# Performance work log

Hardware: AMD Instinct MI355X
Metric: run time of the kernel (lower is better)

The kernel has to match this reference:

```python
import jax, jax.numpy as jnp
import numpy as np

NUM_HEADS = 16
ROPE_THETA = 10000.0


def _rope_angles(seq_len, head_dim, dtype):
    # lucidrains rotary_embedding_torch: freqs = theta^(-2i/d) for i in 0..d/2,
    # angles = pos * freq, then each angle repeated twice along last dim (interleaved pairs).
    inv_freq = 1.0 / (ROPE_THETA ** (jnp.arange(0, head_dim, 2, dtype=jnp.float32) / head_dim))
    angles = jnp.arange(seq_len, dtype=jnp.float32)[:, None] * inv_freq  # [N, D/2]
    return jnp.repeat(angles, 2, axis=-1).astype(dtype)  # [N, D]


def _rotate_half(t):
    # interleaved pairs: (x0, x1) -> (-x1, x0)
    t1 = t[..., ::2]
    t2 = t[..., 1::2]
    return jnp.stack([-t2, t1], axis=-1).reshape(t.shape)


def _apply_rope(t, cos, sin):
    # t: [B, H, N, D]; cos/sin: [N, D]
    return t * cos + _rotate_half(t) * sin


def setup_inputs() -> dict:
    key = jax.random.key(0)
    ks = jax.random.split(key, 5)
    B, N, C = 4, 1024, 1024
    return {
        "x": jax.random.normal(ks[0], (B, N, C), dtype=jnp.float32),
        "w_qkv": jax.random.normal(ks[1], (C, 3 * C), dtype=jnp.float32) * (C ** -0.5),
        "b_qkv": jax.random.normal(ks[2], (3 * C,), dtype=jnp.float32) * 0.02,
        "w_proj": jax.random.normal(ks[3], (C, C), dtype=jnp.float32) * (C ** -0.5),
        "b_proj": jax.random.normal(ks[4], (C,), dtype=jnp.float32) * 0.02,
    }


def reference(x, w_qkv, b_qkv, w_proj, b_proj):
    B, N, C = x.shape
    H = NUM_HEADS
    D = C // H

    qkv = x @ w_qkv + b_qkv  # [B, N, 3C]
    qkv = qkv.reshape(B, N, 3, H, D).transpose(2, 0, 3, 1, 4)  # [3, B, H, N, D]
    q, k, v = qkv[0], qkv[1], qkv[2]

    ang = _rope_angles(N, D, x.dtype)
    cos, sin = jnp.cos(ang), jnp.sin(ang)
    q = _apply_rope(q, cos, sin)
    k = _apply_rope(k, cos, sin)

    scale = D ** -0.5  # SDPA default scale
    scores = jnp.einsum("bhqd,bhkd->bhqk", q, k) * scale
    attn = jax.nn.softmax(scores, axis=-1)
    out = jnp.einsum("bhqk,bhkd->bhqd", attn, v)  # [B, H, N, D]

    out = out.transpose(0, 2, 1, 3).reshape(B, N, C)
    return out @ w_proj + b_proj
```

## Files before the change

### kernel.cpp

```cpp
#include <hip/hip_runtime.h>
#include <math.h>

#define BB 4
#define NN 1024
#define CC 1024
#define HH 16
#define DD 64
#define N3 3072

typedef __attribute__((ext_vector_type(8))) short bf16x8;
typedef __attribute__((ext_vector_type(8))) _Float16 f16x8;
typedef __attribute__((ext_vector_type(4))) _Float16 f16x4;
typedef __attribute__((ext_vector_type(4))) float f32x4;
typedef __attribute__((ext_vector_type(4))) unsigned int u32x4;
typedef __attribute__((ext_vector_type(2))) unsigned int u32x2;

struct ushort4_t { unsigned short x, y, z, w; };

static __device__ __forceinline__ unsigned short f2b(float f) {
    union { float f; unsigned int u; } v; v.f = f;
    unsigned int r = (v.u + 0x7fffu + ((v.u >> 16) & 1u)) >> 16;
    return (unsigned short)r;
}

static __device__ __forceinline__ void ldg_lds16(const void* g, void* l) {
    __builtin_amdgcn_global_load_lds(
        (const __attribute__((address_space(1))) unsigned int*)g,
        (__attribute__((address_space(3))) unsigned int*)l, 16, 0, 0);
}

__global__ __launch_bounds__(256) void prep(const float* __restrict__ x,
                                            const float* __restrict__ wq,
                                            const float* __restrict__ wp,
                                            _Float16* __restrict__ Xh,
                                            _Float16* __restrict__ Wqt,
                                            _Float16* __restrict__ Wpt,
                                            float* __restrict__ ct,
                                            float* __restrict__ st) {
    __shared__ __align__(16) _Float16 T[64][72];
    const int blk = blockIdx.x;
    const int t = threadIdx.x;
    if (blk < 4096) {
        int tid = blk * 256 + t;
        float4 v = ((const float4*)x)[tid];
        f16x4 o = {(_Float16)v.x, (_Float16)v.y, (_Float16)v.z, (_Float16)v.w};
        ((f16x4*)Xh)[tid] = o;
    } else if (blk < 5120) {
        const float* src; _Float16* dst; int ns, k0, n0;
        if (blk < 4864) {
            int idx = blk - 4096;
            k0 = (idx & 15) * 64; n0 = (idx >> 4) * 64;
            src = wq; dst = Wqt; ns = N3;
        } else {
            int idx = blk - 4864;
            k0 = (idx & 15) * 64; n0 = (idx >> 4) * 64;
            src = wp; dst = Wpt; ns = 1024;
        }
        {
            const int r  = t >> 2;
            const int cf = (t & 3) * 16;
            const float* sp = src + (size_t)(k0 + r) * ns + n0 + cf;
            float4 v0 = *(const float4*)(sp);
            float4 v1 = *(const float4*)(sp + 4);
            float4 v2 = *(const float4*)(sp + 8);
            float4 v3 = *(const float4*)(sp + 12);
            f16x8 a, b;
            a[0]=(_Float16)v0.x; a[1]=(_Float16)v0.y; a[2]=(_Float16)v0.z; a[3]=(_Float16)v0.w;
            a[4]=(_Float16)v1.x; a[5]=(_Float16)v1.y; a[6]=(_Float16)v1.z; a[7]=(_Float16)v1.w;
            b[0]=(_Float16)v2.x; b[1]=(_Float16)v2.y; b[2]=(_Float16)v2.z; b[3]=(_Float16)v2.w;
            b[4]=(_Float16)v3.x; b[5]=(_Float16)v3.y; b[6]=(_Float16)v3.z; b[7]=(_Float16)v3.w;
            *(f16x8*)&T[r][cf]     = a;
            *(f16x8*)&T[r][cf + 8] = b;
        }
        __syncthreads();
        {
            const int n  = t >> 2;
            const int kc = t & 3;
            f16x8 o0, o1;
            #pragma unroll
            for (int kk = 0; kk < 8; kk++) o0[kk] = T[kc * 16 + kk][n];
            #pragma unroll
            for (int kk = 0; kk < 8; kk++) o1[kk] = T[kc * 16 + 8 + kk][n];
            _Float16* dp = dst + (size_t)(n0 + n) * 1024 + k0 + kc * 16;
            *(f16x8*)dp       = o0;
            *(f16x8*)(dp + 8) = o1;
        }
    } else {
        int tid = (blk - 5120) * 256 + t;
        int n = tid >> 5, i = tid & 31;
        double ang = (double)n * exp2(-(double)i * (13.287712379549449 / 32.0));
        ct[tid] = (float)cos(ang);
        st[tid] = (float)sin(ang);
    }
}

template<int BM, int BN>
static __device__ __forceinline__ void gemm_body32(const char* gA, const char* gB,
                                                   int m0, int n0,
                                                   _Float16* As0, _Float16* As1,
                                                   _Float16* Bs0, _Float16* Bs1,
                                                   int tid, int ln, int qd,
                                                   int wm, int wn,
                                                   f32x4 (&acc)[BM / 32][BN / 32]) {
    constexpr int PA = BM / 64, PB = BN / 64, MR = BM / 32, NR = BN / 32;
    const int lrow = tid >> 2;
    const int lc   = tid & 3;
    const int swz  = (lc ^ (lrow & 3)) * 8;
    const int rsz  = (qd ^ (ln & 3)) * 8;

    u32x4 pa[PA], pb[PB];

    #pragma unroll
    for (int p = 0; p < PA; p++)
        pa[p] = *(const u32x4*)(gA + (size_t)(m0 + p * 64 + lrow) * 2048 + lc * 16);
    #pragma unroll
    for (int p = 0; p < PB; p++)
        pb[p] = *(const u32x4*)(gB + (size_t)(n0 + p * 64 + lrow) * 2048 + lc * 16);
    #pragma unroll
    for (int p = 0; p < PA; p++) *(u32x4*)&As0[(p * 64 + lrow) * 32 + swz] = pa[p];
    #pragma unroll
    for (int p = 0; p < PB; p++) *(u32x4*)&Bs0[(p * 64 + lrow) * 32 + swz] = pb[p];
    #pragma unroll
    for (int p = 0; p < PA; p++)
        pa[p] = *(const u32x4*)(gA + (size_t)(m0 + p * 64 + lrow) * 2048 + 64 + lc * 16);
    #pragma unroll
    for (int p = 0; p < PB; p++)
        pb[p] = *(const u32x4*)(gB + (size_t)(n0 + p * 64 + lrow) * 2048 + 64 + lc * 16);
    __syncthreads();

    #pragma unroll
    for (int t = 0; t < 32; t++) {
        const _Float16* Ac = (t & 1) ? As1 : As0;
        const _Float16* Bc = (t & 1) ? Bs1 : Bs0;

        f16x8 af[MR], bf[NR];
        #pragma unroll
        for (int i = 0; i < MR; i++)
            af[i] = *(const f16x8*)&Ac[(wm + i * 16 + ln) * 32 + rsz];
        #pragma unroll
        for (int j = 0; j < NR; j++)
            bf[j] = *(const f16x8*)&Bc[(wn + j * 16 + ln) * 32 + rsz];
        #pragma unroll
        for (int i = 0; i < MR; i++)
            #pragma unroll
            for (int j = 0; j < NR; j++)
                acc[i][j] = __builtin_amdgcn_mfma_f32_16x16x32_f16(af[i], bf[j],
                                                                   acc[i][j], 0, 0, 0);

        if (t < 31) {
            _Float16* An = (t & 1) ? As0 : As1;
            _Float16* Bn = (t & 1) ? Bs0 : Bs1;
            #pragma unroll
            for (int p = 0; p < PA; p++) *(u32x4*)&An[(p * 64 + lrow) * 32 + swz] = pa[p];
            #pragma unroll
            for (int p = 0; p < PB; p++) *(u32x4*)&Bn[(p * 64 + lrow) * 32 + swz] = pb[p];
            if (t < 30) {
                size_t ko = (size_t)(t + 2) * 64;
                #pragma unroll
                for (int p = 0; p < PA; p++)
                    pa[p] = *(const u32x4*)(gA + (size_t)(m0 + p * 64 + lrow) * 2048 + ko + lc * 16);
                #pragma unroll
                for (int p = 0; p < PB; p++)
                    pb[p] = *(const u32x4*)(gB + (size_t)(n0 + p * 64 + lrow) * 2048 + ko + lc * 16);
            }
        }
        __syncthreads();
    }
}

static __device__ __forceinline__ void gemm_body_pipe_n64(const char* gA, const char* gB,
                                                          int m0, int n0,
                                                          _Float16* As0, _Float16* As1,
                                                          _Float16* Bs0, _Float16* Bs1,
                                                          int tid, int ln, int qd,
                                                          int wm, int wn, f32x4 acc[4][2]) {
    const int lrow   = tid >> 3;
    const int lchunk = tid & 7;
    const int swz    = (lchunk ^ (lrow & 7)) * 8;

    u32x4 pa[4], pb[2];

    #pragma unroll
    for (int c = 0; c < 4; c++)
        pa[c] = *(const u32x4*)(gA + (size_t)(m0 + c * 32 + lrow) * 2048 + lchunk * 16);
    #pragma unroll
    for (int c = 0; c < 2; c++)
        pb[c] = *(const u32x4*)(gB + (size_t)(n0 + c * 32 + lrow) * 2048 + lchunk * 16);
    #pragma unroll
    for (int c = 0; c < 4; c++)
        *(u32x4*)&As0[(c * 32 + lrow) * 64 + swz] = pa[c];
    #pragma unroll
    for (int c = 0; c < 2; c++)
        *(u32x4*)&Bs0[(c * 32 + lrow) * 64 + swz] = pb[c];
    #pragma unroll
    for (int c = 0; c < 4; c++)
        pa[c] = *(const u32x4*)(gA + (size_t)(m0 + c * 32 + lrow) * 2048 + 128 + lchunk * 16);
    #pragma unroll
    for (int c = 0; c < 2; c++)
        pb[c] = *(const u32x4*)(gB + (size_t)(n0 + c * 32 + lrow) * 2048 + 128 + lchunk * 16);
    __syncthreads();

    #pragma unroll
    for (int t = 0; t < 16; t++) {
        const _Float16* Ac = (t & 1) ? As1 : As0;
        const _Float16* Bc = (t & 1) ? Bs1 : Bs0;

        #pragma unroll
        for (int kc = 0; kc < 2; kc++) {
            f16x8 af[4], bf[2];
            #pragma unroll
            for (int i = 0; i < 4; i++)
                af[i] = *(const f16x8*)&Ac[(wm + i * 16 + ln) * 64 +
                                           (((kc * 4 + qd) ^ (ln & 7)) * 8)];
            #pragma unroll
            for (int j = 0; j < 2; j++)
                bf[j] = *(const f16x8*)&Bc[(wn + j * 16 + ln) * 64 +
                                           (((kc * 4 + qd) ^ (ln & 7)) * 8)];
            #pragma unroll
            for (int i = 0; i < 4; i++)
                #pragma unroll
                for (int j = 0; j < 2; j++)
                    acc[i][j] = __builtin_amdgcn_mfma_f32_16x16x32_f16(af[i], bf[j],
                                                                       acc[i][j], 0, 0, 0);
        }

        if (t < 15) {
            _Float16* An = (t & 1) ? As0 : As1;
            _Float16* Bn = (t & 1) ? Bs0 : Bs1;
            #pragma unroll
            for (int c = 0; c < 4; c++)
                *(u32x4*)&An[(c * 32 + lrow) * 64 + swz] = pa[c];
            #pragma unroll
            for (int c = 0; c < 2; c++)
                *(u32x4*)&Bn[(c * 32 + lrow) * 64 + swz] = pb[c];
            if (t < 14) {
                size_t ko = (size_t)(t + 2) * 128;
                #pragma unroll
                for (int c = 0; c < 4; c++)
                    pa[c] = *(const u32x4*)(gA + (size_t)(m0 + c * 32 + lrow) * 2048 + ko + lchunk * 16);
                #pragma unroll
                for (int c = 0; c < 2; c++)
                    pb[c] = *(const u32x4*)(gB + (size_t)(n0 + c * 32 + lrow) * 2048 + ko + lchunk * 16);
            }
        }
        __syncthreads();
    }
}

__global__ __launch_bounds__(256, 3) void qkv_mfma(const _Float16* __restrict__ Ah,
                                                   const _Float16* __restrict__ Bt,
                                                   const float* __restrict__ bias,
                                                   const float* __restrict__ cost,
                                                   const float* __restrict__ sint,
                                                   unsigned short* __restrict__ Q,
                                                   unsigned short* __restrict__ K,
                                                   unsigned short* __restrict__ Vtg) {
    __shared__ __align__(16) _Float16 As[2][128 * 32];
    __shared__ __align__(16) _Float16 Bs[2][128 * 32];
    const int t = threadIdx.x;
    const int lane = t & 63;
    const int w = t >> 6;
    const int ln = lane & 15, qd = lane >> 4;
    const int n0 = blockIdx.x * 128;
    const int m0 = blockIdx.y * 128;
    const int wm = (w >> 1) * 64, wn = (w & 1) * 64;

    f32x4 acc[4][4];
    #pragma unroll
    for (int i = 0; i < 4; i++)
        #pragma unroll
        for (int j = 0; j < 4; j++) acc[i][j] = (f32x4){0.f, 0.f, 0.f, 0.f};

    gemm_body32<128, 128>((const char*)Ah, (const char*)Bt, m0, n0,
                          As[0], As[1], Bs[0], Bs[1], t, ln, qd, wm, wn, acc);

    const int s = n0 >> 10;
    const int h = ((n0 + wn) >> 6) & 15;
    if (s < 2) {
        unsigned short* dst = (s == 0) ? Q : K;
        const float sc0 = (s == 0) ? 0.125f : 1.0f;
        #pragma unroll
        for (int i = 0; i < 4; i++) {
            #pragma unroll
            for (int reg = 0; reg < 4; reg++) {
                int row = m0 + wm + i * 16 + qd * 4 + reg;
                int b = row >> 10, n = row & 1023;
                size_t obase = (((size_t)(b * HH + h)) * NN + n) * DD;
                #pragma unroll
                for (int j = 0; j < 4; j++) {
                    int d = j * 16 + ln;
                    float v = acc[i][j][reg] + bias[n0 + wn + d];
                    float pv = __shfl_xor(v, 1);
                    float cs = cost[n * 32 + (d >> 1)];
                    float sn = sint[n * 32 + (d >> 1)];
                    float outv = ((d & 1) ? (v * cs + pv * sn) : (v * cs - pv * sn)) * sc0;
                    dst[obase + d] = f2b(outv);
                }
            }
        }
    } else {
        #pragma unroll
        for (int i = 0; i < 4; i++) {
            int row0 = m0 + wm + i * 16 + qd * 4;
            int b = row0 >> 10, n = row0 & 1023;
            size_t tbase = ((size_t)(b * HH + h)) * DD * NN + n;
            #pragma unroll
            for (int j = 0; j < 4; j++) {
                int d = j * 16 + ln;
                float bb = bias[n0 + wn + d];
                ushort4_t pk;
                pk.x = f2b(acc[i][j][0] + bb);
                pk.y = f2b(acc[i][j][1] + bb);
                pk.z = f2b(acc[i][j][2] + bb);
                pk.w = f2b(acc[i][j][3] + bb);
                *(ushort4_t*)&Vtg[tbase + (size_t)d * NN] = pk;
            }
        }
    }
}

__global__ __launch_bounds__(256) void attn_flash(const unsigned short* __restrict__ Qb,
                                                  const unsigned short* __restrict__ Kb,
                                                  const unsigned short* __restrict__ Vtg,
                                                  _Float16* __restrict__ AO) {
    __shared__ __align__(16) unsigned short Ks[3][64 * 64];
    __shared__ __align__(16) unsigned short Vt[2][64 * 64];
    __shared__ __align__(16) unsigned short Ps[4][32 * 64];

    const int t    = threadIdx.x;
    const int lane = t & 63;
    const int w    = t >> 6;
    const int ln   = lane & 15;
    const int qd   = lane >> 4;
    const int bq   = blockIdx.x;
    const int h    = blockIdx.y;
    const int b    = blockIdx.z;
    const size_t base = (size_t)(b * HH + h) * NN * DD;
    const char* Kc = (const char*)(Kb + base);
    const char* Vc = (const char*)(Vtg + base);
    const int xorc = ((lane & 7) ^ (lane >> 3)) * 16;
    const int r8   = lane >> 3;
    const int wrow = w * 16;

    bf16x8 qf[2][2];
    #pragma unroll
    for (int g = 0; g < 2; g++) {
        const unsigned short* qp = Qb + base +
            (size_t)(bq * 128 + w * 32 + g * 16 + ln) * DD + qd * 8;
        qf[g][0] = *(const bf16x8*)qp;
        qf[g][1] = *(const bf16x8*)(qp + 32);
    }

    f32x4 o[2][5];
    #pragma unroll
    for (int g = 0; g < 2; g++)
        #pragma unroll
        for (int x = 0; x < 5; x++) o[g][x] = (f32x4){0.f, 0.f, 0.f, 0.f};

    bf16x8 onesf;
    #pragma unroll
    for (int x = 0; x < 8; x++) onesf[x] = (short)0x3F80;

    #pragma unroll
    for (int tile = 0; tile < 3; tile++)
        #pragma unroll
        for (int c = 0; c < 2; c++) {
            int rr = wrow + c * 8 + r8;
            ldg_lds16(Kc + (size_t)(tile * 64 + rr) * 128 + xorc,
                      &Ks[tile][(wrow + c * 8) * 64]);
        }
    #pragma unroll
    for (int tile = 0; tile < 2; tile++)
        #pragma unroll
        for (int c = 0; c < 2; c++) {
            int rr = wrow + c * 8 + r8;
            ldg_lds16(Vc + (size_t)rr * 2048 + (size_t)tile * 128 + xorc,
                      &Vt[tile][(wrow + c * 8) * 64]);
        }
    __syncthreads();

    f32x4 scur[2][4];
    {
        const unsigned short* KsB = Ks[0];
        #pragma unroll
        for (int j = 0; j < 4; j++) {
            bf16x8 k0f = *(const bf16x8*)&KsB[(ln + 16 * j) * 64 + ((qd ^ (ln & 7)) * 8)];
            bf16x8 k1f = *(const bf16x8*)&KsB[(ln + 16 * j) * 64 + (((4 + qd) ^ (ln & 7)) * 8)];
            #pragma unroll
            for (int g = 0; g < 2; g++) {
                f32x4 sj = {0.f, 0.f, 0.f, 0.f};
                sj = __builtin_amdgcn_mfma_f32_16x16x32_bf16(k0f, qf[g][0], sj, 0, 0, 0);
                sj = __builtin_amdgcn_mfma_f32_16x16x32_bf16(k1f, qf[g][1], sj, 0, 0, 0);
                scur[g][j] = sj;
            }
        }
    }

    const float C1 = 1.44269504f;
    const float C0 = -16.0f * 1.44269504f;
    const int swp = 2 * (ln & 7);

    #pragma unroll
    for (int tt = 0; tt < 16; tt++) {
        f32x4 snext[2][4];
        if (tt < 15) {
            const unsigned short* KsB = Ks[(tt + 1) % 3];
            #pragma unroll
            for (int j = 0; j < 4; j++) {
                bf16x8 k0f = *(const bf16x8*)&KsB[(ln + 16 * j) * 64 + ((qd ^ (ln & 7)) * 8)];
                bf16x8 k1f = *(const bf16x8*)&KsB[(ln + 16 * j) * 64 + (((4 + qd) ^ (ln & 7)) * 8)];
                #pragma unroll
                for (int g = 0; g < 2; g++) {
                    f32x4 sj = {0.f, 0.f, 0.f, 0.f};
                    sj = __builtin_amdgcn_mfma_f32_16x16x32_bf16(k0f, qf[g][0], sj, 0, 0, 0);
                    sj = __builtin_amdgcn_mfma_f32_16x16x32_bf16(k1f, qf[g][1], sj, 0, 0, 0);
                    snext[g][j] = sj;
                }
            }
        }

        unsigned short* PsB = &Ps[w][0];
        #pragma unroll
        for (int g = 0; g < 2; g++) {
            char* rowp = (char*)PsB + (g * 16 + ln) * 128;
            #pragma unroll
            for (int j = 0; j < 4; j++) {
                float p0 = exp2f(fmaf(scur[g][j][0], C1, C0));
                float p1 = exp2f(fmaf(scur[g][j][1], C1, C0));
                float p2 = exp2f(fmaf(scur[g][j][2], C1, C0));
                float p3 = exp2f(fmaf(scur[g][j][3], C1, C0));
                unsigned int lo, hi;
                asm("v_cvt_pk_bf16_f32 %0, %1, %2" : "=v"(lo) : "v"(p0), "v"(p1));
                asm("v_cvt_pk_bf16_f32 %0, %1, %2" : "=v"(hi) : "v"(p2), "v"(p3));
                u32x2 pk; pk[0] = lo; pk[1] = hi;
                *(u32x2*)(rowp + (((4 * j + qd) ^ swp) * 8)) = pk;
            }
        }

        {
            const unsigned short* VtB = Vt[tt & 1];
            bf16x8 pf[2][2];
            #pragma unroll
            for (int g = 0; g < 2; g++) {
                pf[g][0] = *(const bf16x8*)&PsB[(g * 16 + ln) * 64 + ((qd ^ (ln & 7)) * 8)];
                pf[g][1] = *(const bf16x8*)&PsB[(g * 16 + ln) * 64 + (((4 + qd) ^ (ln & 7)) * 8)];
            }
            #pragma unroll
            for (int j = 0; j < 4; j++) {
                bf16x8 v0f = *(const bf16x8*)&VtB[(ln + 16 * j) * 64 + ((qd ^ (ln & 7)) * 8)];
                bf16x8 v1f = *(const bf16x8*)&VtB[(ln + 16 * j) * 64 + (((4 + qd) ^ (ln & 7)) * 8)];
                #pragma unroll
                for (int g = 0; g < 2; g++) {
                    o[g][j] = __builtin_amdgcn_mfma_f32_16x16x32_bf16(pf[g][0], v0f, o[g][j], 0, 0, 0);
                    o[g][j] = __builtin_amdgcn_mfma_f32_16x16x32_bf16(pf[g][1], v1f, o[g][j], 0, 0, 0);
                }
            }
            #pragma unroll
            for (int g = 0; g < 2; g++) {
                o[g][4] = __builtin_amdgcn_mfma_f32_16x16x32_bf16(pf[g][0], onesf, o[g][4], 0, 0, 0);
                o[g][4] = __builtin_amdgcn_mfma_f32_16x16x32_bf16(pf[g][1], onesf, o[g][4], 0, 0, 0);
            }
        }

        __syncthreads();

        if (tt <= 12) {
            int tile = tt + 3;
            #pragma unroll
            for (int c = 0; c < 2; c++) {
                int rr = wrow + c * 8 + r8;
                ldg_lds16(Kc + (size_t)(tile * 64 + rr) * 128 + xorc,
                          &Ks[tt % 3][(wrow + c * 8) * 64]);
            }
        }
        if (tt <= 13) {
            int tile = tt + 2;
            #pragma unroll
            for (int c = 0; c < 2; c++) {
                int rr = wrow + c * 8 + r8;
                ldg_lds16(Vc + (size_t)rr * 2048 + (size_t)tile * 128 + xorc,
                          &Vt[tt & 1][(wrow + c * 8) * 64]);
            }
        }

        #pragma unroll
        for (int g = 0; g < 2; g++)
            #pragma unroll
            for (int j = 0; j < 4; j++) scur[g][j] = snext[g][j];
    }

    #pragma unroll
    for (int g = 0; g < 2; g++)
        #pragma unroll
        for (int r = 0; r < 4; r++) {
            float inv = 1.0f / o[g][4][r];
            int q = bq * 128 + w * 32 + g * 16 + qd * 4 + r;
            _Float16* op = AO + (((size_t)b * NN + q) * HH + h) * DD + ln;
            op[0]  = (_Float16)(o[g][0][r] * inv);
            op[16] = (_Float16)(o[g][1][r] * inv);
            op[32] = (_Float16)(o[g][2][r] * inv);
            op[48] = (_Float16)(o[g][3][r] * inv);
        }
}

__global__ __launch_bounds__(256) void proj_mfma(const _Float16* __restrict__ Ah,
                                                 const _Float16* __restrict__ Bt,
                                                 const float* __restrict__ bias,
                                                 float* __restrict__ out) {
    __shared__ __align__(16) _Float16 As[2][128 * 64];
    __shared__ __align__(16) _Float16 Bs[2][64 * 64];
    const int t = threadIdx.x;
    const int lane = t & 63;
    const int w = t >> 6;
    const int ln = lane & 15, qd = lane >> 4;
    const int n0 = blockIdx.x * 64;
    const int m0 = blockIdx.y * 128;
    const int wm = (w >> 1) * 64, wn = (w & 1) * 32;

    f32x4 acc[4][2];
    #pragma unroll
    for (int i = 0; i < 4; i++)
        #pragma unroll
        for (int j = 0; j < 2; j++) acc[i][j] = (f32x4){0.f, 0.f, 0.f, 0.f};

    gemm_body_pipe_n64((const char*)Ah, (const char*)Bt, m0, n0,
                       As[0], As[1], Bs[0], Bs[1], t, ln, qd, wm, wn, acc);

    #pragma unroll
    for (int i = 0; i < 4; i++) {
        #pragma unroll
        for (int reg = 0; reg < 4; reg++) {
            int row = m0 + wm + i * 16 + qd * 4 + reg;
            #pragma unroll
            for (int j = 0; j < 2; j++) {
                int col = n0 + wn + j * 16 + ln;
                out[(size_t)row * 1024 + col] = acc[i][j][reg] + bias[col];
            }
        }
    }
}

extern "C" void kernel_launch(void* const* d_in, const int* in_sizes, int n_in,
                              void* d_out, int out_size, void* d_ws, size_t ws_size,
                              hipStream_t stream) {
    const float* x      = (const float*)d_in[0];
    const float* w_qkv  = (const float*)d_in[1];
    const float* b_qkv  = (const float*)d_in[2];
    const float* w_proj = (const float*)d_in[3];
    const float* b_proj = (const float*)d_in[4];
    float* out = (float*)d_out;

    char* ws = (char*)d_ws;
    _Float16* Xh   = (_Float16*)(ws);
    _Float16* Wqt  = (_Float16*)(ws + (8u << 20));
    _Float16* Wpt  = (_Float16*)(ws + (14u << 20));
    unsigned short* Q  = (unsigned short*)(ws + (16u << 20));
    unsigned short* K  = (unsigned short*)(ws + (24u << 20));
    unsigned short* Vt = (unsigned short*)(ws + (32u << 20));
    _Float16* AOh  = (_Float16*)(ws + (40u << 20));
    float* cost    = (float*)(ws + (48u << 20));
    float* sint    = (float*)(ws + (48u << 20) + (128u << 10));

    prep<<<5248, 256, 0, stream>>>(x, w_qkv, w_proj, Xh, Wqt, Wpt, cost, sint);
    qkv_mfma<<<dim3(24, 32), 256, 0, stream>>>(Xh, Wqt, b_qkv, cost, sint, Q, K, Vt);
    attn_flash<<<dim3(8, 16, 4), 256, 0, stream>>>(Q, K, Vt, AOh);
    proj_mfma<<<dim3(16, 32), 256, 0, stream>>>(AOh, Wpt, b_proj, out);
}
```

Before: 178.8 us.

## Rewrite QKV GEMM with 256x256 tiles and 4-stage direct-to-LDS pipeline

Replaces the register-staged double-buffered 128x128 QKV GEMM with a 512-thread, 256x256 tile kernel. Global loads now go straight into LDS through global_load_lds across a 4-slot ring, with explicit vmcnt/lgkmcnt waits, raw s_barrier, and setprio around the MFMA bursts. The aim is more operand reuse per block and better overlap of loads with compute. In exchange it uses much more LDS and more registers (128 accumulators per thread), and launches only 192 blocks, which could leave CUs idle and relies on hand-written wait counts being correct.

Result: no change. 177.0 us (-1.0%).

```diff
diff --git a/kernel.cpp b/kernel.cpp
--- a/kernel.cpp
+++ b/kernel.cpp
@@ -28,6 +28,14 @@
         (const __attribute__((address_space(1))) unsigned int*)g,
         (__attribute__((address_space(3))) unsigned int*)l, 16, 0, 0);
 }
+
+static __device__ __forceinline__ void barx()  { asm volatile("s_barrier" ::: "memory"); }
+static __device__ __forceinline__ void wlg0()  { asm volatile("s_waitcnt lgkmcnt(0)" ::: "memory");
+                                                 __builtin_amdgcn_sched_barrier(0); }
+static __device__ __forceinline__ void wvm8()  { asm volatile("s_waitcnt vmcnt(8)" ::: "memory"); }
+static __device__ __forceinline__ void wvm4()  { asm volatile("s_waitcnt vmcnt(4)" ::: "memory"); }
+static __device__ __forceinline__ void wvm0()  { asm volatile("s_waitcnt vmcnt(0)" ::: "memory"); }
+static __device__ __forceinline__ void wnone() {}
 
 __global__ __launch_bounds__(256) void prep(const float* __restrict__ x,
                                             const float* __restrict__ wq,
@@ -94,160 +102,7 @@
     }
 }
 
-template<int BM, int BN>
-static __device__ __forceinline__ void gemm_body32(const char* gA, const char* gB,
-                                                   int m0, int n0,
-                                                   _Float16* As0, _Float16* As1,
-                                                   _Float16* Bs0, _Float16* Bs1,
-                                                   int tid, int ln, int qd,
-                                                   int wm, int wn,
-                                                   f32x4 (&acc)[BM / 32][BN / 32]) {
-    constexpr int PA = BM / 64, PB = BN / 64, MR = BM / 32, NR = BN / 32;
-    const int lrow = tid >> 2;
-    const int lc   = tid & 3;
-    const int swz  = (lc ^ (lrow & 3)) * 8;
-    const int rsz  = (qd ^ (ln & 3)) * 8;
-
-    u32x4 pa[PA], pb[PB];
-
-    #pragma unroll
-    for (int p = 0; p < PA; p++)
-        pa[p] = *(const u32x4*)(gA + (size_t)(m0 + p * 64 + lrow) * 2048 + lc * 16);
-    #pragma unroll
-    for (int p = 0; p < PB; p++)
-        pb[p] = *(const u32x4*)(gB + (size_t)(n0 + p * 64 + lrow) * 2048 + lc * 16);
-    #pragma unroll
-    for (int p = 0; p < PA; p++) *(u32x4*)&As0[(p * 64 + lrow) * 32 + swz] = pa[p];
-    #pragma unroll
-    for (int p = 0; p < PB; p++) *(u32x4*)&Bs0[(p * 64 + lrow) * 32 + swz] = pb[p];
-    #pragma unroll
-    for (int p = 0; p < PA; p++)
-        pa[p] = *(const u32x4*)(gA + (size_t)(m0 + p * 64 + lrow) * 2048 + 64 + lc * 16);
-    #pragma unroll
-    for (int p = 0; p < PB; p++)
-        pb[p] = *(const u32x4*)(gB + (size_t)(n0 + p * 64 + lrow) * 2048 + 64 + lc * 16);
-    __syncthreads();
-
-    #pragma unroll
-    for (int t = 0; t < 32; t++) {
-        const _Float16* Ac = (t & 1) ? As1 : As0;
-        const _Float16* Bc = (t & 1) ? Bs1 : Bs0;
-
-        f16x8 af[MR], bf[NR];
-        #pragma unroll
-        for (int i = 0; i < MR; i++)
-            af[i] = *(const f16x8*)&Ac[(wm + i * 16 + ln) * 32 + rsz];
-        #pragma unroll
-        for (int j = 0; j < NR; j++)
-            bf[j] = *(const f16x8*)&Bc[(wn + j * 16 + ln) * 32 + rsz];
-        #pragma unroll
-        for (int i = 0; i < MR; i++)
-            #pragma unroll
-            for (int j = 0; j < NR; j++)
-                acc[i][j] = __builtin_amdgcn_mfma_f32_16x16x32_f16(af[i], bf[j],
-                                                                   acc[i][j], 0, 0, 0);
-
-        if (t < 31) {
-            _Float16* An = (t & 1) ? As0 : As1;
-            _Float16* Bn = (t & 1) ? Bs0 : Bs1;
-            #pragma unroll
-            for (int p = 0; p < PA; p++) *(u32x4*)&An[(p * 64 + lrow) * 32 + swz] = pa[p];
-            #pragma unroll
-            for (int p = 0; p < PB; p++) *(u32x4*)&Bn[(p * 64 + lrow) * 32 + swz] = pb[p];
-            if (t < 30) {
-                size_t ko = (size_t)(t + 2) * 64;
-                #pragma unroll
-                for (int p = 0; p < PA; p++)
-                    pa[p] = *(const u32x4*)(gA + (size_t)(m0 + p * 64 + lrow) * 2048 + ko + lc * 16);
-                #pragma unroll
-                for (int p = 0; p < PB; p++)
-                    pb[p] = *(const u32x4*)(gB + (size_t)(n0 + p * 64 + lrow) * 2048 + ko + lc * 16);
-            }
-        }
-        __syncthreads();
-    }
-}
-
-static __device__ __forceinline__ void gemm_body_pipe_n64(const char* gA, const char* gB,
-                                                          int m0, int n0,
-                                                          _Float16* As0, _Float16* As1,
-                                                          _Float16* Bs0, _Float16* Bs1,
-                                                          int tid, int ln, int qd,
-                                                          int wm, int wn, f32x4 acc[4][2]) {
-    const int lrow   = tid >> 3;
-    const int lchunk = tid & 7;
-    const int swz    = (lchunk ^ (lrow & 7)) * 8;
-
-    u32x4 pa[4], pb[2];
-
-    #pragma unroll
-    for (int c = 0; c < 4; c++)
-        pa[c] = *(const u32x4*)(gA + (size_t)(m0 + c * 32 + lrow) * 2048 + lchunk * 16);
-    #pragma unroll
-    for (int c = 0; c < 2; c++)
-        pb[c] = *(const u32x4*)(gB + (size_t)(n0 + c * 32 + lrow) * 2048 + lchunk * 16);
-    #pragma unroll
-    for (int c = 0; c < 4; c++)
-        *(u32x4*)&As0[(c * 32 + lrow) * 64 + swz] = pa[c];
-    #pragma unroll
-    for (int c = 0; c < 2; c++)
-        *(u32x4*)&Bs0[(c * 32 + lrow) * 64 + swz] = pb[c];
-    #pragma unroll
-    for (int c = 0; c < 4; c++)
-        pa[c] = *(const u32x4*)(gA + (size_t)(m0 + c * 32 + lrow) * 2048 + 128 + lchunk * 16);
-    #pragma unroll
-    for (int c = 0; c < 2; c++)
-        pb[c] = *(const u32x4*)(gB + (size_t)(n0 + c * 32 + lrow) * 2048 + 128 + lchunk * 16);
-    __syncthreads();
-
-    #pragma unroll
-    for (int t = 0; t < 16; t++) {
-        const _Float16* Ac = (t & 1) ? As1 : As0;
-        const _Float16* Bc = (t & 1) ? Bs1 : Bs0;
-
-        #pragma unroll
-        for (int kc = 0; kc < 2; kc++) {
-            f16x8 af[4], bf[2];
-            #pragma unroll
-            for (int i = 0; i < 4; i++)
-                af[i] = *(const f16x8*)&Ac[(wm + i * 16 + ln) * 64 +
-                                           (((kc * 4 + qd) ^ (ln & 7)) * 8)];
-            #pragma unroll
-            for (int j = 0; j < 2; j++)
-                bf[j] = *(const f16x8*)&Bc[(wn + j * 16 + ln) * 64 +
-                                           (((kc * 4 + qd) ^ (ln & 7)) * 8)];
-            #pragma unroll
-            for (int i = 0; i < 4; i++)
-                #pragma unroll
-                for (int j = 0; j < 2; j++)
-                    acc[i][j] = __builtin_amdgcn_mfma_f32_16x16x32_f16(af[i], bf[j],
-                                                                       acc[i][j], 0, 0, 0);
-        }
-
-        if (t < 15) {
-            _Float16* An = (t & 1) ? As0 : As1;
-            _Float16* Bn = (t & 1) ? Bs0 : Bs1;
-            #pragma unroll
-            for (int c = 0; c < 4; c++)
-                *(u32x4*)&An[(c * 32 + lrow) * 64 + swz] = pa[c];
-            #pragma unroll
-            for (int c = 0; c < 2; c++)
-                *(u32x4*)&Bn[(c * 32 + lrow) * 64 + swz] = pb[c];
-            if (t < 14) {
-                size_t ko = (size_t)(t + 2) * 128;
-                #pragma unroll
-                for (int c = 0; c < 4; c++)
-                    pa[c] = *(const u32x4*)(gA + (size_t)(m0 + c * 32 + lrow) * 2048 + ko + lchunk * 16);
-                #pragma unroll
-                for (int c = 0; c < 2; c++)
-                    pb[c] = *(const u32x4*)(gB + (size_t)(n0 + c * 32 + lrow) * 2048 + ko + lchunk * 16);
-            }
-        }
-        __syncthreads();
-    }
-}
-
-__global__ __launch_bounds__(256, 3) void qkv_mfma(const _Float16* __restrict__ Ah,
+__global__ __launch_bounds__(512, 2) void qkv_mfma(const _Float16* __restrict__ Ah,
                                                    const _Float16* __restrict__ Bt,
                                                    const float* __restrict__ bias,
                                                    const float* __restrict__ cost,
@@ -255,32 +110,103 @@
                                                    unsigned short* __restrict__ Q,
                                                    unsigned short* __restrict__ K,
                                                    unsigned short* __restrict__ Vtg) {
-    __shared__ __align__(16) _Float16 As[2][128 * 32];
-    __shared__ __align__(16) _Float16 Bs[2][128 * 32];
-    const int t = threadIdx.x;
+    __shared__ __align__(16) _Float16 LA[4][128 * 64];
+    __shared__ __align__(16) _Float16 LB[4][128 * 64];
+
+    const int t    = threadIdx.x;
     const int lane = t & 63;
-    const int w = t >> 6;
-    const int ln = lane & 15, qd = lane >> 4;
-    const int n0 = blockIdx.x * 128;
-    const int m0 = blockIdx.y * 128;
-    const int wm = (w >> 1) * 64, wn = (w & 1) * 64;
-
-    f32x4 acc[4][4];
-    #pragma unroll
-    for (int i = 0; i < 4; i++)
+    const int w    = t >> 6;
+    const int ln   = lane & 15, qd = lane >> 4;
+    const int n0   = blockIdx.x * 256;
+    const int m0   = blockIdx.y * 256;
+    const int wm   = (w >> 2) * 128;
+    const int wn   = (w & 3) * 64;
+
+    const int L0 = t >> 3, hc0 = (t & 7) ^ (L0 & 7);
+    const int row0 = 2 * L0 + (hc0 >> 2), co0 = (hc0 & 3) * 16;
+    const int pp = 512 + t;
+    const int L1 = pp >> 3, hc1 = (pp & 7) ^ (L1 & 7);
+    const int row1 = 2 * L1 + (hc1 >> 2), co1 = (hc1 & 3) * 16;
+
+    const char* gA = (const char*)Ah;
+    const char* gB = (const char*)Bt;
+    const size_t aof0 = (size_t)(m0 + row0) * 2048 + co0;
+    const size_t aof1 = (size_t)(m0 + row1) * 2048 + co1;
+    const size_t bof0 = (size_t)(n0 + row0) * 2048 + co0;
+    const size_t bof1 = (size_t)(n0 + row1) * 2048 + co1;
+    const int ld0 = (w * 64) * 8;
+    const int ld1 = (512 + w * 64) * 8;
+
+#define STAGE_A(kk, SLOT) { ldg_lds16(gA + aof0 + (size_t)(kk) * 64, &LA[SLOT][ld0]); \
+                            ldg_lds16(gA + aof1 + (size_t)(kk) * 64, &LA[SLOT][ld1]); }
+#define STAGE_B(kk, SLOT) { ldg_lds16(gB + bof0 + (size_t)(kk) * 64, &LB[SLOT][ld0]); \
+                            ldg_lds16(gB + bof1 + (size_t)(kk) * 64, &LB[SLOT][ld1]); }
+
+    STAGE_A(0, 0); STAGE_B(0, 0);
+    STAGE_A(1, 1); STAGE_B(1, 1);
+    STAGE_A(2, 2); STAGE_B(2, 2);
+    wvm8();
+    barx();
+
+    f32x4 acc[8][4];
+    #pragma unroll
+    for (int i = 0; i < 8; i++)
         #pragma unroll
         for (int j = 0; j < 4; j++) acc[i][j] = (f32x4){0.f, 0.f, 0.f, 0.f};
 
-    gemm_body32<128, 128>((const char*)Ah, (const char*)Bt, m0, n0,
-                          As[0], As[1], Bs[0], Bs[1], t, ln, qd, wm, wn, acc);
-
-    const int s = n0 >> 10;
+    auto frag = [&](const _Float16* Lb, int r, int c) -> f16x8 {
+        int idx = ((r >> 1) << 6) + ((((((r & 1) << 2) | c)) ^ ((r >> 1) & 7)) << 3);
+        return *(const f16x8*)&Lb[idx];
+    };
+
+#define QK_TILE(kk, SLOT, STG, WAITFN) {                                            \
+    const _Float16* Ab = LA[SLOT];                                                  \
+    const _Float16* Bb = LB[SLOT];                                                  \
+    f16x8 af[4], bf[4];                                                             \
+    _Pragma("unroll") for (int i = 0; i < 4; i++) af[i] = frag(Ab, wm + i * 16 + ln, qd); \
+    _Pragma("unroll") for (int j = 0; j < 4; j++) bf[j] = frag(Bb, wn + j * 16 + ln, qd); \
+    if (STG) STAGE_A((kk) + 3, ((kk) + 3) & 3);                                     \
+    barx(); wlg0();                                                                 \
+    __builtin_amdgcn_s_setprio(1);                                                  \
+    _Pragma("unroll") for (int i = 0; i < 4; i++)                                   \
+        _Pragma("unroll") for (int j = 0; j < 4; j++)                               \
+            acc[i][j] = __builtin_amdgcn_mfma_f32_16x16x32_f16(af[i], bf[j], acc[i][j], 0, 0, 0); \
+    __builtin_amdgcn_s_setprio(0);                                                  \
+    barx();                                                                         \
+    _Pragma("unroll") for (int i = 0; i < 4; i++) af[i] = frag(Ab, wm + 64 + i * 16 + ln, qd); \
+    if (STG) STAGE_B((kk) + 3, ((kk) + 3) & 3);                                     \
+    WAITFN();                                                                       \
+    barx(); wlg0();                                                                 \
+    __builtin_amdgcn_s_setprio(1);                                                  \
+    _Pragma("unroll") for (int i = 0; i < 4; i++)                                   \
+        _Pragma("unroll") for (int j = 0; j < 4; j++)                               \
+            acc[4 + i][j] = __builtin_amdgcn_mfma_f32_16x16x32_f16(af[i], bf[j], acc[4 + i][j], 0, 0, 0); \
+    __builtin_amdgcn_s_setprio(0);                                                  \
+    barx();                                                                         \
+}
+
+    for (int k = 0; k < 28; k += 4) {
+        QK_TILE(k + 0, 0, 1, wvm8);
+        QK_TILE(k + 1, 1, 1, wvm8);
+        QK_TILE(k + 2, 2, 1, wvm8);
+        QK_TILE(k + 3, 3, 1, wvm8);
+    }
+    QK_TILE(28, 0, 1, wvm8);
+    QK_TILE(29, 1, 0, wvm4);
+    QK_TILE(30, 2, 0, wvm0);
+    QK_TILE(31, 3, 0, wnone);
+
+#undef QK_TILE
+#undef STAGE_A
+#undef STAGE_B
+
+    const int s = (n0 + wn) >> 10;
     const int h = ((n0 + wn) >> 6) & 15;
     if (s < 2) {
         unsigned short* dst = (s == 0) ? Q : K;
         const float sc0 = (s == 0) ? 0.125f : 1.0f;
         #pragma unroll
-        for (int i = 0; i < 4; i++) {
+        for (int i = 0; i < 8; i++) {
             #pragma unroll
             for (int reg = 0; reg < 4; reg++) {
                 int row = m0 + wm + i * 16 + qd * 4 + reg;
@@ -300,9 +226,9 @@
         }
     } else {
         #pragma unroll
-        for (int i = 0; i < 4; i++) {
-            int row0 = m0 + wm + i * 16 + qd * 4;
-            int b = row0 >> 10, n = row0 & 1023;
+        for (int i = 0; i < 8; i++) {
+            int row0v = m0 + wm + i * 16 + qd * 4;
+            int b = row0v >> 10, n = row0v & 1023;
             size_t tbase = ((size_t)(b * HH + h)) * DD * NN + n;
             #pragma unroll
             for (int j = 0; j < 4; j++) {
@@ -316,6 +242,85 @@
                 *(ushort4_t*)&Vtg[tbase + (size_t)d * NN] = pk;
             }
         }
+    }
+}
+
+static __device__ __forceinline__ void gemm_body_pipe_n64(const char* gA, const char* gB,
+                                                          int m0, int n0,
+                                                          _Float16* As0, _Float16* As1,
+                                                          _Float16* Bs0, _Float16* Bs1,
+                                                          int tid, int ln, int qd,
+                                                          int wm, int wn, f32x4 acc[4][2]) {
+    const int lrow   = tid >> 3;
+    const int lchunk = tid & 7;
+    const int swz    = (lchunk ^ (lrow & 7)) * 8;
+
+    u32x4 pa[4], pb[2];
+
+    #pragma unroll
+    for (int c = 0; c < 4; c++)
+        pa[c] = *(const u32x4*)(gA + (size_t)(m0 + c * 32 + lrow) * 2048 + lchunk * 16);
+    #pragma unroll
+    for (int c = 0; c < 2; c++)
+        pb[c] = *(const u32x4*)(gB + (size_t)(n0 + c * 32 + lrow) * 2048 + lchunk * 16);
+    #pragma unroll
+    for (int c = 0; c < 4; c++)
+        *(u32x4*)&As0[(c * 32 + lrow) * 64 + swz] = pa[c];
+    #pragma unroll
+    for (int c = 0; c < 2; c++)
+        *(u32x4*)&Bs0[(c * 32 + lrow) * 64 + swz] = pb[c];
+    #pragma unroll
+    for (int c = 0; c < 4; c++)
+        pa[c] = *(const u32x4*)(gA + (size_t)(m0 + c * 32 + lrow) * 2048 + 128 + lchunk * 16);
+    #pragma unroll
+    for (int c = 0; c < 2; c++)
+        pb[c] = *(const u32x4*)(gB + (size_t)(n0 + c * 32 + lrow) * 2048 + 128 + lchunk * 16);
+    __syncthreads();
+
+    #pragma unroll
+    for (int t = 0; t < 16; t++) {
+        const _Float16* Ac = (t & 1) ? As1 : As0;
+        const _Float16* Bc = (t & 1) ? Bs1 : Bs0;
+
+        #pragma unroll
+        for (int kc = 0; kc < 2; kc++) {
+            f16x8 af[4], bf[2];
+            #pragma unroll
+            for (int i = 0; i < 4; i++)
+                af[i] = *(const f16x8*)&Ac[(wm + i * 16 + ln) * 64 +
+                                           (((kc * 4 + qd) ^ (ln & 7)) * 8)];
+            #pragma unroll
+            for (int j = 0; j < 2; j++)
+                bf[j] = *(const f16x8*)&Bc[(wn + j * 16 + ln) * 64 +
+                                           (((kc * 4 + qd) ^ (ln & 7)) * 8)];
+            #pragma unroll
+            for (int i = 0; i < 4; i++)
+                #pragma unroll
+                for (int j = 0; j < 2; j++)
+                    acc[i][j] = __builtin_amdgcn_mfma_f32_16x16x32_f16(af[i], bf[j],
+                                                                       acc[i][j], 0, 0, 0);
+        }
+
+        if (t < 15) {
+            _Float16* An = (t & 1) ? As0 : As1;
+            _Float16* Bn = (t & 1) ? Bs0 : Bs1;
+            #pragma unroll
+            for (int c = 0; c < 4; c++)
+                *(u32x4*)&An[(c * 32 + lrow) * 64 + swz] = pa[c];
+            #pragma unroll
+            for (int c = 0; c < 2; c++)
+                *(u32x4*)&Bn[(c * 32 + lrow) * 64 + swz] = pb[c];
+            if (t < 14) {
+                size_t ko = (size_t)(t + 2) * 128;
+                #pragma unroll
+                for (int c = 0; c < 4; c++)
+                    pa[c] = *(const u32x4*)(gA + (size_t)(m0 + c * 32 + lrow) * 2048 + ko + lchunk * 16);
+                #pragma unroll
+                for (int c = 0; c < 2; c++)
+                    pb[c] = *(const u32x4*)(gB + (size_t)(n0 + c * 32 + lrow) * 2048 + ko + lchunk * 16);
+            }
+        }
+        __syncthreads();
     }
 }
 
@@ -562,7 +567,7 @@
     float* sint    = (float*)(ws + (48u << 20) + (128u << 10));
 
     prep<<<5248, 256, 0, stream>>>(x, w_qkv, w_proj, Xh, Wqt, Wpt, cost, sint);
-    qkv_mfma<<<dim3(24, 32), 256, 0, stream>>>(Xh, Wqt, b_qkv, cost, sint, Q, K, Vt);
+    qkv_mfma<<<dim3(12, 16), 512, 0, stream>>>(Xh, Wqt, b_qkv, cost, sint, Q, K, Vt);
     attn_flash<<<dim3(8, 16, 4), 256, 0, stream>>>(Q, K, Vt, AOh);
     proj_mfma<<<dim3(16, 32), 256, 0, stream>>>(AOh, Wpt, b_proj, out);
 }
```
